# Kernel tuning notes

Hardware: AMD Instinct MI355X
Metric: run time of the kernel (lower is better)

## Reference

```python
import jax, jax.numpy as jnp
import numpy as np

B, S, HID = 2, 2048, 2048
NH, HD = 16, 128
EPS = 1e-5
ROPE_BASE = 10000.0


def setup_inputs() -> dict:
    key = jax.random.key(0)
    k1, k2, k3 = jax.random.split(key, 3)
    std = 1.0 / np.sqrt(HID)
    x = jax.random.normal(k1, (B, S, HID), jnp.float32)
    w_in = jax.random.truncated_normal(k2, -3.0, 3.0, (3 * NH * HD, HID), jnp.float32) * std
    std_o = std / np.sqrt(2.0)  # layer_id = 0 -> std / sqrt(2*(0+1))
    w_out = jax.random.truncated_normal(k3, -3.0, 3.0, (HID, NH * HD), jnp.float32) * std_o
    q_norm_w = jnp.ones((NH * HD,), jnp.float32)
    k_norm_w = jnp.ones((NH * HD,), jnp.float32)
    return {"x": x, "w_in": w_in, "w_out": w_out, "q_norm_w": q_norm_w, "k_norm_w": k_norm_w}


def _rms_norm(x, w, eps=EPS):
    ms = jnp.mean(x * x, axis=-1, keepdims=True)
    return x * jax.lax.rsqrt(ms + eps) * w


def _rope(x, offset=0):
    # x: [B, S, NH, HD]; rotate-half convention
    half = HD // 2
    inv_freq = 1.0 / (ROPE_BASE ** (jnp.arange(half, dtype=jnp.float32) / half))
    pos = jnp.arange(x.shape[1], dtype=jnp.float32) + offset
    ang = pos[:, None] * inv_freq                      # [S, half]
    cos = jnp.cos(ang)[None, :, None, :]
    sin = jnp.sin(ang)[None, :, None, :]
    x1, x2 = jnp.split(x, 2, axis=-1)
    return jnp.concatenate([x1 * cos - x2 * sin, x2 * cos + x1 * sin], axis=-1)


def reference(x, w_in, w_out, q_norm_w, k_norm_w):
    b, s, _ = x.shape
    qkv = jnp.einsum('bsh,oh->bso', x, w_in)           # [B, S, 3*NH*HD]
    q, k, v = jnp.split(qkv, 3, axis=-1)
    # qk-norm over the flat (NH*HD) axis, as in the torch module
    q = _rms_norm(q, q_norm_w)
    k = _rms_norm(k, k_norm_w)
    q = q.reshape(b, s, NH, HD)
    k = k.reshape(b, s, NH, HD)
    v = v.reshape(b, s, NH, HD)
    q = _rope(q)
    k = _rope(k)
    scale = 1.0 / np.sqrt(HD)
    scores = jnp.einsum('bqhd,bkhd->bhqk', q, k) * scale
    causal = jnp.tril(jnp.ones((s, s), dtype=bool))
    scores = jnp.where(causal[None, None, :, :], scores, jnp.finfo(scores.dtype).min)
    probs = jax.nn.softmax(scores, axis=-1)
    out = jnp.einsum('bhqk,bkhd->bqhd', probs, v).reshape(b, s, NH * HD)
    return jnp.einsum('bso,ho->bsh', out, w_out)
```

## Files before the change

### kernel.cpp

```cpp
#include <hip/hip_runtime.h>
#include <hip/hip_bf16.h>
#include <math.h>

#define B_   2
#define S_   2048
#define HID_ 2048
#define NH_  16
#define HD_  128
#define QKV_ (3 * NH_ * HD_)
#define EPS_ 1e-5f

typedef __bf16 bf16x8 __attribute__((ext_vector_type(8)));
typedef __bf16 bf16x4 __attribute__((ext_vector_type(4)));
typedef __bf16 bf16x2 __attribute__((ext_vector_type(2)));
typedef float  f32x4  __attribute__((ext_vector_type(4)));

__global__ __launch_bounds__(256) void cast3_f32_bf16(
    const float* __restrict__ a, __bf16* __restrict__ ao, int na4,
    const float* __restrict__ b, __bf16* __restrict__ bo, int nb4,
    const float* __restrict__ c, __bf16* __restrict__ co, int nc4) {
    int j = blockIdx.x * 256 + threadIdx.x;
    const float* src;
    __bf16* dst;
    if (j < na4) {
        src = a; dst = ao;
    } else {
        j -= na4;
        if (j < nb4) {
            src = b; dst = bo;
        } else {
            j -= nb4;
            if (j >= nc4) return;
            src = c; dst = co;
        }
    }
    float4 v = reinterpret_cast<const float4*>(src)[j];
    bf16x4 o = {(__bf16)v.x, (__bf16)v.y, (__bf16)v.z, (__bf16)v.w};
    reinterpret_cast<bf16x4*>(dst)[j] = o;
}

__device__ __forceinline__ void gload_lds16(const __bf16* g, __bf16* l) {
    __builtin_amdgcn_global_load_lds(
        (const __attribute__((address_space(1))) void*)g,
        (__attribute__((address_space(3))) void*)l, 16, 0, 0);
}

template <typename OutT>
__global__ __launch_bounds__(256) void gemm_bt_mfma(
    const __bf16* __restrict__ A, const __bf16* __restrict__ Bm,
    OutT* __restrict__ C, int M, int N, int K) {
    __shared__ __bf16 As[128 * 32];
    __shared__ __bf16 Bs[128 * 32];

    const int tid  = threadIdx.x;
    const int w    = tid >> 6;
    const int lane = tid & 63;
    const int wh   = w >> 1;
    const int ww   = w & 1;
    const int lrow = lane & 15;
    const int quad = lane >> 4;
    const int m0 = blockIdx.y * 128;
    const int n0 = blockIdx.x * 128;

    f32x4 acc[4][4] = {};

    for (int k0 = 0; k0 < K; k0 += 32) {
        __syncthreads();
#pragma unroll
        for (int t = 0; t < 2; ++t) {
            int c   = (w * 2 + t) * 64 + lane;
            int row = c >> 2;
            int kc  = (c & 3) * 8;
            gload_lds16(&A[(size_t)(m0 + row) * K + k0 + kc],
                        &As[(w * 2 + t) * 512]);
            gload_lds16(&Bm[(size_t)(n0 + row) * K + k0 + kc],
                        &Bs[(w * 2 + t) * 512]);
        }
        __syncthreads();

        bf16x8 af[4], bf[4];
#pragma unroll
        for (int i = 0; i < 4; ++i)
            af[i] = *reinterpret_cast<const bf16x8*>(
                &As[(wh * 64 + i * 16 + lrow) * 32 + quad * 8]);
#pragma unroll
        for (int j = 0; j < 4; ++j)
            bf[j] = *reinterpret_cast<const bf16x8*>(
                &Bs[(ww * 64 + j * 16 + lrow) * 32 + quad * 8]);
#pragma unroll
        for (int i = 0; i < 4; ++i)
#pragma unroll
            for (int j = 0; j < 4; ++j)
                acc[i][j] = __builtin_amdgcn_mfma_f32_16x16x32_bf16(
                    af[i], bf[j], acc[i][j], 0, 0, 0);
    }

#pragma unroll
    for (int i = 0; i < 4; ++i) {
#pragma unroll
        for (int r = 0; r < 4; ++r) {
            int row = m0 + wh * 64 + i * 16 + quad * 4 + r;
            size_t base = (size_t)row * N + n0 + ww * 64 + lrow;
#pragma unroll
            for (int j = 0; j < 4; ++j) {
                float v = acc[i][j][r];
                C[base + j * 16] = (OutT)v;
            }
        }
    }
}

__global__ __launch_bounds__(256) void normrope_kernel(
    __bf16* __restrict__ qkv, const float* __restrict__ qw,
    const float* __restrict__ kw) {
    const int row = blockIdx.x;
    const int sel = blockIdx.y;
    const int pos = row & (S_ - 1);
    __bf16* p = qkv + (size_t)row * QKV_ + sel * 2048;
    const float* w = sel ? kw : qw;

    __shared__ float buf[2048];
    __shared__ float red[4];
    const int tid = threadIdx.x;
    const int e   = tid * 8;

    bf16x8 t = *reinterpret_cast<const bf16x8*>(&p[e]);
    float xs[8];
    float ss = 0.f;
#pragma unroll
    for (int u = 0; u < 8; ++u) {
        xs[u] = (float)t[u];
        buf[e + u] = xs[u];
        ss += xs[u] * xs[u];
    }
#pragma unroll
    for (int off = 32; off > 0; off >>= 1) ss += __shfl_xor(ss, off, 64);
    if ((tid & 63) == 0) red[tid >> 6] = ss;
    __syncthreads();
    float total = red[0] + red[1] + red[2] + red[3];
    float scale = rsqrtf(total * (1.f / 2048.f) + EPS_);

    const float kfreq2 = -0.20762050593046f;
    const int jbase = e & 63;
    const bool first = (e & 127) < 64;
    const int ep = e ^ 64;

    float ps[8], ws[8], pw[8];
#pragma unroll
    for (int u = 0; u < 8; ++u) ps[u] = buf[ep + u];
    float4 w0 = *reinterpret_cast<const float4*>(&w[e]);
    float4 w1 = *reinterpret_cast<const float4*>(&w[e + 4]);
    float4 p0 = *reinterpret_cast<const float4*>(&w[ep]);
    float4 p1 = *reinterpret_cast<const float4*>(&w[ep + 4]);
    ws[0]=w0.x; ws[1]=w0.y; ws[2]=w0.z; ws[3]=w0.w;
    ws[4]=w1.x; ws[5]=w1.y; ws[6]=w1.z; ws[7]=w1.w;
    pw[0]=p0.x; pw[1]=p0.y; pw[2]=p0.z; pw[3]=p0.w;
    pw[4]=p1.x; pw[5]=p1.y; pw[6]=p1.z; pw[7]=p1.w;

    bf16x8 o8;
#pragma unroll
    for (int u = 0; u < 8; ++u) {
        float inv_freq = exp2f((float)(jbase + u) * kfreq2);
        float ang = (float)pos * inv_freq;
        float sn = __sinf(ang);
        float cs = __cosf(ang);
        float a  = xs[u] * scale * ws[u];
        float bb = ps[u] * scale * pw[u];
        float o  = first ? (a * cs - bb * sn) : (a * cs + bb * sn);
        o8[u] = (__bf16)o;
    }
    *reinterpret_cast<bf16x8*>(&p[e]) = o8;
}

#define VTP 36

__global__ __launch_bounds__(512, 4) void attn_mfma(
    const __bf16* __restrict__ qkv, __bf16* __restrict__ aout) {
    const int flat = (int)blockIdx.x;
    const int vid  = (flat & 7) * 64 + (flat >> 3);
    const int bh   = vid >> 4;
    const int qt   = 15 - (vid & 15);
    const int b    = bh >> 4;
    const int h    = bh & (NH_ - 1);
    const int q0   = qt * 128;
    const int tid  = threadIdx.x;
    const int w    = tid >> 6;
    const int lane = tid & 63;
    const int lrow = lane & 15;
    const int quad = lane >> 4;

    __shared__ __bf16 Ks[2][4][32 * 32];
    __shared__ __bf16 Vt[2][128 * VTP];
    __shared__ __bf16 Pb[8][16 * VTP];

    const size_t base = (size_t)(b * S_) * QKV_ + (size_t)h * HD_;
    const int qrow = q0 + w * 16 + lrow;

    bf16x8 qf[4];
#pragma unroll
    for (int kc = 0; kc < 4; ++kc)
        qf[kc] = *reinterpret_cast<const bf16x8*>(
            &qkv[base + (size_t)qrow * QKV_ + kc * 32 + quad * 8]);

    f32x4 o[8] = {};
    float lpart = 0.f;

    const int ktmax_w   = 4 * qt + (w >> 1);
    const int ktmax_blk = 4 * qt + 3;
    const float sl2 = 0.12751743671f;

    const __bf16* kg0 = qkv + base + 2048 +
                        (size_t)((w & 1) * 16 + (lane >> 2)) * QKV_ +
                        (w >> 1) * 32 + (lane & 3) * 8;
    const int g  = tid >> 4;
    const int kp = tid & 15;
    const __bf16* vg0 = qkv + base + 4096 + (size_t)(kp * 2) * QKV_ + g * 8;

    gload_lds16(kg0, &Ks[0][w >> 1][(w & 1) * 512]);
    bf16x8 v0 = {}, v1 = {};
    if (tid < 256) {
        v0 = *reinterpret_cast<const bf16x8*>(vg0);
        v1 = *reinterpret_cast<const bf16x8*>(vg0 + QKV_);
    }

    for (int kt = 0; kt <= ktmax_blk; ++kt) {
        const int buf = kt & 1;
        if (tid < 256) {
#pragma unroll
            for (int u = 0; u < 8; ++u) {
                bf16x2 pr = {v0[u], v1[u]};
                *reinterpret_cast<bf16x2*>(
                    &Vt[buf][(g * 8 + u) * VTP + kp * 2]) = pr;
            }
        }
        __syncthreads();
        if (kt < ktmax_blk) {
            const __bf16* kg = kg0 + (size_t)(kt + 1) * 32 * QKV_;
            gload_lds16(kg, &Ks[buf ^ 1][w >> 1][(w & 1) * 512]);
            if (tid < 256) {
                const __bf16* vg = vg0 + (size_t)(kt + 1) * 32 * QKV_;
                v0 = *reinterpret_cast<const bf16x8*>(vg);
                v1 = *reinterpret_cast<const bf16x8*>(vg + QKV_);
            }
        }
        if (kt <= ktmax_w) {
            f32x4 sc[2] = {};
            __builtin_amdgcn_s_setprio(1);
#pragma unroll
            for (int kc = 0; kc < 4; ++kc) {
                bf16x8 kf0 = *reinterpret_cast<const bf16x8*>(
                    &Ks[buf][kc][lrow * 32 + quad * 8]);
                bf16x8 kf1 = *reinterpret_cast<const bf16x8*>(
                    &Ks[buf][kc][(16 + lrow) * 32 + quad * 8]);
                sc[0] = __builtin_amdgcn_mfma_f32_16x16x32_bf16(
                    kf0, qf[kc], sc[0], 0, 0, 0);
                sc[1] = __builtin_amdgcn_mfma_f32_16x16x32_bf16(
                    kf1, qf[kc], sc[1], 0, 0, 0);
            }
            __builtin_amdgcn_s_setprio(0);
            const bool diag = (kt == ktmax_w);
            float p[2][4];
#pragma unroll
            for (int m2 = 0; m2 < 2; ++m2)
#pragma unroll
                for (int r = 0; r < 4; ++r) {
                    float s = sc[m2][r] * sl2 - 32.f;
                    if (diag && kt * 32 + m2 * 16 + quad * 4 + r > qrow)
                        s = -1e30f;
                    p[m2][r] = exp2f(s);
                    lpart += p[m2][r];
                }
#pragma unroll
            for (int m2 = 0; m2 < 2; ++m2) {
                bf16x4 pb = {(__bf16)p[m2][0], (__bf16)p[m2][1],
                             (__bf16)p[m2][2], (__bf16)p[m2][3]};
                *reinterpret_cast<bf16x4*>(
                    &Pb[w][lrow * VTP + m2 * 16 + quad * 4]) = pb;
            }
            bf16x8 pf = *reinterpret_cast<const bf16x8*>(
                &Pb[w][lrow * VTP + quad * 8]);
            __builtin_amdgcn_s_setprio(1);
#pragma unroll
            for (int dt = 0; dt < 8; ++dt) {
                bf16x8 vf = *reinterpret_cast<const bf16x8*>(
                    &Vt[buf][(dt * 16 + lrow) * VTP + quad * 8]);
                o[dt] = __builtin_amdgcn_mfma_f32_16x16x32_bf16(
                    vf, pf, o[dt], 0, 0, 0);
            }
            __builtin_amdgcn_s_setprio(0);
        }
    }

    lpart += __shfl_xor(lpart, 16, 64);
    lpart += __shfl_xor(lpart, 32, 64);
    const float invl = 1.f / lpart;
    const size_t orow = (size_t)(b * S_ + qrow) * (NH_ * HD_) + (size_t)h * HD_;
#pragma unroll
    for (int dt = 0; dt < 8; ++dt) {
        bf16x4 ov = {(__bf16)(o[dt][0] * invl), (__bf16)(o[dt][1] * invl),
                     (__bf16)(o[dt][2] * invl), (__bf16)(o[dt][3] * invl)};
        *reinterpret_cast<bf16x4*>(&aout[orow + dt * 16 + quad * 4]) = ov;
    }
}

extern "C" void kernel_launch(void* const* d_in, const int* in_sizes, int n_in,
                              void* d_out, int out_size, void* d_ws,
                              size_t ws_size, hipStream_t stream) {
    const float* x     = (const float*)d_in[0];
    const float* w_in  = (const float*)d_in[1];
    const float* w_out = (const float*)d_in[2];
    const float* qw    = (const float*)d_in[3];
    const float* kw    = (const float*)d_in[4];
    float* out = (float*)d_out;

    const int M = B_ * S_;
    char* ws = (char*)d_ws;
    __bf16* qkv_b   = (__bf16*)(ws);
    __bf16* w_out_b = (__bf16*)(ws + (size_t)50331648);
    __bf16* x_b     = (__bf16*)(ws + (size_t)58720256);
    __bf16* attn_b  = x_b;
    __bf16* w_in_b  = (__bf16*)(ws + (size_t)75497472);

    dim3 blk(256);

    {
        const int na4 = (M * HID_) / 4;
        const int nb4 = (QKV_ * HID_) / 4;
        const int nc4 = (HID_ * NH_ * HD_) / 4;
        const int tot = na4 + nb4 + nc4;
        cast3_f32_bf16<<<dim3((tot + 255) / 256), blk, 0, stream>>>(
            x, x_b, na4, w_in, w_in_b, nb4, w_out, w_out_b, nc4);
    }

    gemm_bt_mfma<__bf16><<<dim3(QKV_ / 128, M / 128), blk, 0, stream>>>(
        x_b, w_in_b, qkv_b, M, QKV_, HID_);
    normrope_kernel<<<dim3(M, 2), blk, 0, stream>>>(qkv_b, qw, kw);
    attn_mfma<<<dim3((S_ / 128) * B_ * NH_), dim3(512), 0, stream>>>(
        qkv_b, attn_b);
    gemm_bt_mfma<float><<<dim3(HID_ / 128, M / 128), blk, 0, stream>>>(
        attn_b, w_out_b, out, M, HID_, NH_ * HD_);
}
```

Baseline: 440.7 us.

## Rewrite projection GEMMs as triple-buffered 128x256 tile kernel with swizzled LDS

```diff
diff --git a/kernel.cpp b/kernel.cpp
--- a/kernel.cpp
+++ b/kernel.cpp
@@ -45,67 +45,111 @@
         (__attribute__((address_space(3))) void*)l, 16, 0, 0);
 }
 
+__device__ __forceinline__ void stage_tile6(
+    const __bf16* pA, const __bf16* pB, __bf16* buf, int w, int K) {
+#pragma unroll
+    for (int s = 0; s < 2; ++s)
+        gload_lds16(pA + (size_t)s * 64 * K, buf + s * 4096 + w * 512);
+#pragma unroll
+    for (int s = 0; s < 4; ++s)
+        gload_lds16(pB + (size_t)s * 64 * K, buf + 8192 + s * 4096 + w * 512);
+}
+
 template <typename OutT>
-__global__ __launch_bounds__(256) void gemm_bt_mfma(
+__global__ __launch_bounds__(512, 2) void gemm_bt_8ph(
     const __bf16* __restrict__ A, const __bf16* __restrict__ Bm,
     OutT* __restrict__ C, int M, int N, int K) {
-    __shared__ __bf16 As[128 * 32];
-    __shared__ __bf16 Bs[128 * 32];
+    __shared__ __bf16 lds[3][24576];
 
     const int tid  = threadIdx.x;
     const int w    = tid >> 6;
     const int lane = tid & 63;
-    const int wh   = w >> 1;
-    const int ww   = w & 1;
     const int lrow = lane & 15;
     const int quad = lane >> 4;
-    const int m0 = blockIdx.y * 128;
-    const int n0 = blockIdx.x * 128;
-
+    const int wm   = w >> 2;
+    const int wn   = w & 3;
+
+    const int chunk = (int)gridDim.x >> 3;
+    const int flat  = (int)blockIdx.x;
+    const int vid   = (flat & 7) * chunk + (flat >> 3);
+    const int by    = vid & 31;
+    const int bx    = vid >> 5;
+    const int m0 = by * 128;
+    const int n0 = bx * 256;
+
+    const int lr = lane >> 3;
+    const int lg = lane & 7;
+    const __bf16* pA = A  + (size_t)(m0 + w * 8 + lr) * K + ((lg ^ lr) << 3);
+    const __bf16* pB = Bm + (size_t)(n0 + w * 8 + lr) * K + ((lg ^ lr) << 3);
+
+    const int nt = K >> 6;
     f32x4 acc[4][4] = {};
 
-    for (int k0 = 0; k0 < K; k0 += 32) {
-        __syncthreads();
-#pragma unroll
-        for (int t = 0; t < 2; ++t) {
-            int c   = (w * 2 + t) * 64 + lane;
-            int row = c >> 2;
-            int kc  = (c & 3) * 8;
-            gload_lds16(&A[(size_t)(m0 + row) * K + k0 + kc],
-                        &As[(w * 2 + t) * 512]);
-            gload_lds16(&Bm[(size_t)(n0 + row) * K + k0 + kc],
-                        &Bs[(w * 2 + t) * 512]);
-        }
-        __syncthreads();
-
-        bf16x8 af[4], bf[4];
-#pragma unroll
-        for (int i = 0; i < 4; ++i)
-            af[i] = *reinterpret_cast<const bf16x8*>(
-                &As[(wh * 64 + i * 16 + lrow) * 32 + quad * 8]);
-#pragma unroll
-        for (int j = 0; j < 4; ++j)
-            bf[j] = *reinterpret_cast<const bf16x8*>(
-                &Bs[(ww * 64 + j * 16 + lrow) * 32 + quad * 8]);
-#pragma unroll
-        for (int i = 0; i < 4; ++i)
+    stage_tile6(pA, pB, &lds[0][0], w, K);
+    stage_tile6(pA + 64, pB + 64, &lds[1][0], w, K);
+
+    int cur = 0;
+    for (int t = 0; t < nt; ++t) {
+        __bf16* bufc = &lds[cur][0];
+        int nxt = cur + 2; if (nxt >= 3) nxt -= 3;
+        if (t + 2 < nt) {
+            stage_tile6(pA + (size_t)(t + 2) * 64, pB + (size_t)(t + 2) * 64,
+                        &lds[nxt][0], w, K);
+            asm volatile("s_waitcnt vmcnt(12)" ::: "memory");
+        } else if (t + 1 < nt) {
+            asm volatile("s_waitcnt vmcnt(6)" ::: "memory");
+        } else {
+            asm volatile("s_waitcnt vmcnt(0)" ::: "memory");
+        }
+        __builtin_amdgcn_s_barrier();
+        asm volatile("" ::: "memory");
+
+#pragma unroll
+        for (int q = 0; q < 2; ++q) {
+            bf16x8 af[2][2], bfv[4][2];
+#pragma unroll
+            for (int i = 0; i < 2; ++i)
+#pragma unroll
+                for (int kk = 0; kk < 2; ++kk)
+                    af[i][kk] = *reinterpret_cast<const bf16x8*>(
+                        &bufc[(wm * 64 + (q * 2 + i) * 16 + lrow) * 64 +
+                              (((kk * 4 + quad) ^ (lrow & 7)) << 3)]);
 #pragma unroll
             for (int j = 0; j < 4; ++j)
-                acc[i][j] = __builtin_amdgcn_mfma_f32_16x16x32_bf16(
-                    af[i], bf[j], acc[i][j], 0, 0, 0);
-    }
-
-#pragma unroll
-    for (int i = 0; i < 4; ++i) {
+#pragma unroll
+                for (int kk = 0; kk < 2; ++kk)
+                    bfv[j][kk] = *reinterpret_cast<const bf16x8*>(
+                        &bufc[8192 + (wn * 64 + j * 16 + lrow) * 64 +
+                              (((kk * 4 + quad) ^ (lrow & 7)) << 3)]);
+            __builtin_amdgcn_s_barrier();
+            asm volatile("" ::: "memory");
+            __builtin_amdgcn_s_setprio(1);
+#pragma unroll
+            for (int i = 0; i < 2; ++i)
+#pragma unroll
+                for (int j = 0; j < 4; ++j)
+#pragma unroll
+                    for (int kk = 0; kk < 2; ++kk)
+                        acc[q * 2 + i][j] =
+                            __builtin_amdgcn_mfma_f32_16x16x32_bf16(
+                                af[i][kk], bfv[j][kk], acc[q * 2 + i][j],
+                                0, 0, 0);
+            __builtin_amdgcn_s_setprio(0);
+        }
+        __builtin_amdgcn_s_barrier();
+        asm volatile("" ::: "memory");
+        cur = (cur == 2) ? 0 : cur + 1;
+    }
+
+#pragma unroll
+    for (int mi = 0; mi < 4; ++mi) {
 #pragma unroll
         for (int r = 0; r < 4; ++r) {
-            int row = m0 + wh * 64 + i * 16 + quad * 4 + r;
-            size_t base = (size_t)row * N + n0 + ww * 64 + lrow;
-#pragma unroll
-            for (int j = 0; j < 4; ++j) {
-                float v = acc[i][j][r];
-                C[base + j * 16] = (OutT)v;
-            }
+            int row = m0 + wm * 64 + mi * 16 + quad * 4 + r;
+            size_t basec = (size_t)row * N + n0 + wn * 64 + lrow;
+#pragma unroll
+            for (int nj = 0; nj < 4; ++nj)
+                C[basec + nj * 16] = (OutT)acc[mi][nj][r];
         }
     }
 }
@@ -332,11 +376,11 @@
             x, x_b, na4, w_in, w_in_b, nb4, w_out, w_out_b, nc4);
     }
 
-    gemm_bt_mfma<__bf16><<<dim3(QKV_ / 128, M / 128), blk, 0, stream>>>(
-        x_b, w_in_b, qkv_b, M, QKV_, HID_);
+    gemm_bt_8ph<__bf16><<<dim3((M / 128) * (QKV_ / 256)), dim3(512), 0,
+                          stream>>>(x_b, w_in_b, qkv_b, M, QKV_, HID_);
     normrope_kernel<<<dim3(M, 2), blk, 0, stream>>>(qkv_b, qw, kw);
     attn_mfma<<<dim3((S_ / 128) * B_ * NH_), dim3(512), 0, stream>>>(
         qkv_b, attn_b);
-    gemm_bt_mfma<float><<<dim3(HID_ / 128, M / 128), blk, 0, stream>>>(
-        attn_b, w_out_b, out, M, HID_, NH_ * HD_);
-}
+    gemm_bt_8ph<float><<<dim3((M / 128) * (HID_ / 256)), dim3(512), 0,
+                         stream>>>(attn_b, w_out_b, out, M, HID_, NH_ * HD_);
+}
```

Result: faster. 417.0 us (-5.4%).
